# Performance work log

Hardware: AMD Instinct MI355X
Metric: run time of the kernel (lower is better)

The kernel has to match this reference:

```python
import jax, jax.numpy as jnp
import numpy as np

N, E, F_IN, F_E, H, HEADS, NG = 50000, 300000, 16, 8, 64, 4, 64
D_HEAD = H // HEADS
EPS = 1e-5


def setup_inputs() -> dict:
    key = jax.random.key(0)
    ks = jax.random.split(key, 12)
    def rn(k, shape, s=0.1):
        return jax.random.normal(k, shape, jnp.float32) * s
    return dict(
        x=jax.random.normal(ks[0], (N, F_IN), jnp.float32),
        edge_index=jax.random.randint(ks[1], (2, E), 0, N),
        edge_attr=jax.random.normal(ks[2], (E, F_E), jnp.float32),
        batch=jnp.sort(jax.random.randint(ks[3], (N,), 0, NG)),
        # edge_net: Linear(F_E, H*F_IN) -> ReLU -> Linear(H*F_IN, H*F_IN)
        en_w1=rn(ks[4], (F_E, H * F_IN)), en_b1=jnp.zeros((H * F_IN,), jnp.float32),
        en_w2=rn(ks[5], (H * F_IN, H * F_IN)), en_b2=jnp.zeros((H * F_IN,), jnp.float32),
        # NNConv root weight + bias
        root_w=rn(ks[6], (F_IN, H)), conv1_b=jnp.zeros((H,), jnp.float32),
        norm1_w=jnp.ones((H,), jnp.float32), norm1_b=jnp.zeros((H,), jnp.float32),
        # GATConv: lin weight, attention vectors, bias
        gat_w=rn(ks[7], (H, H)),
        att_src=rn(ks[8], (HEADS, D_HEAD)), att_dst=rn(ks[9], (HEADS, D_HEAD)),
        gat_b=jnp.zeros((H,), jnp.float32),
        norm2_w=jnp.ones((H,), jnp.float32), norm2_b=jnp.zeros((H,), jnp.float32),
        lin_w=rn(ks[10], (H, 1)), lin_b=jnp.zeros((1,), jnp.float32),
    )


def _graph_layernorm(x, w, b):
    # PyG LayerNorm(mode='graph') with batch=None: scalar mean/std over ALL elems
    mu = x.mean()
    sd = jnp.sqrt(((x - mu) ** 2).mean())
    return (x - mu) / (sd + EPS) * w + b


def reference(x, edge_index, edge_attr, batch, en_w1, en_b1, en_w2, en_b2,
              root_w, conv1_b, norm1_w, norm1_b, gat_w, att_src, att_dst,
              gat_b, norm2_w, norm2_b, lin_w, lin_b):
    src, dst = edge_index[0], edge_index[1]
    # --- NNConv: per-edge weight matrices from edge_net ---
    w_e = jax.nn.relu(edge_attr @ en_w1 + en_b1) @ en_w2 + en_b2
    w_e = w_e.reshape(E, F_IN, H)                      # [E, in, out]
    msg = jnp.einsum('ef,efh->eh', x[src], w_e)        # gather-matmul per edge
    agg = jax.ops.segment_sum(msg, dst, num_segments=N)
    deg = jax.ops.segment_sum(jnp.ones((E,), x.dtype), dst, num_segments=N)
    agg = agg / jnp.maximum(deg, 1.0)[:, None]         # aggr='mean'
    h = x @ root_w + agg + conv1_b
    h = jax.nn.relu(h)
    h = _graph_layernorm(h, norm1_w, norm1_b)
    # dropout: eval mode -> identity
    # --- GATConv (edge_attr=None at call site; add self-loops, softmax attn) ---
    loops = jnp.arange(N)
    s2 = jnp.concatenate([src, loops])
    d2 = jnp.concatenate([dst, loops])
    xh = (h @ gat_w).reshape(N, HEADS, D_HEAD)
    a_src = (xh * att_src).sum(-1)                     # [N, HEADS]
    a_dst = (xh * att_dst).sum(-1)
    alpha = jax.nn.leaky_relu(a_src[s2] + a_dst[d2], 0.2)  # [E+N, HEADS]
    amax = jax.ops.segment_max(alpha, d2, num_segments=N)
    alpha = jnp.exp(alpha - amax[d2])
    asum = jax.ops.segment_sum(alpha, d2, num_segments=N)
    alpha = alpha / (asum[d2] + 1e-16)
    out = jax.ops.segment_sum(alpha[:, :, None] * xh[s2], d2, num_segments=N)
    h2 = out.reshape(N, H) + gat_b                     # concat heads
    h2 = jax.nn.relu(h2)
    h2 = _graph_layernorm(h2, norm2_w, norm2_b)
    # --- global mean pool + linear head ---
    gs = jax.ops.segment_sum(h2, batch, num_segments=NG)
    cnt = jax.ops.segment_sum(jnp.ones((N,), h2.dtype), batch, num_segments=NG)
    pooled = gs / jnp.maximum(cnt, 1.0)[:, None]
    return pooled @ lin_w + lin_b                      # [NG, 1]
```

## Files before the change

### kernel.cpp

```cpp
#include <hip/hip_runtime.h>
#include <hip/hip_bf16.h>

#define N_NODES 50000
#define E_EDGES 300000
#define NGRAPH 64
#define NCHUNK 129
#define CSPLIT 65
#define NKG 1034
#define NEGRP 1172
#define LNEPS 1e-5f
#define NBLK_N 196
#define NBLK_P 12500
#define RPRE16 1.00048828125f

typedef _Float16 f16x8 __attribute__((ext_vector_type(8)));
typedef _Float16 f16x2 __attribute__((ext_vector_type(2)));
typedef float floatx16 __attribute__((ext_vector_type(16)));
typedef float f32x2 __attribute__((ext_vector_type(2)));
typedef unsigned int u32x4 __attribute__((ext_vector_type(4)));

__device__ __forceinline__ void async_load16(const void* g, void* l) {
  __builtin_amdgcn_global_load_lds(
      (__attribute__((address_space(1))) void*)g,
      (__attribute__((address_space(3))) void*)l, 16, 0, 0);
}

__global__ void k_prep(const float* __restrict__ w2, const float* __restrict__ b2,
                       _Float16* __restrict__ Tt3) {
  __shared__ float tile[32][65];
  int t = threadIdx.x;
  int kg0 = blockIdx.x * 2;
  int kf0 = kg0 * 16;
  int kfr = t >> 6;
  int n0 = t & 63;
#pragma unroll
  for (int it = 0; it < 8; ++it) {
    int kfl = it * 4 + kfr;
    int kf = kf0 + kfl;
    float v = 0.f;
    if (kf < 16384) v = w2[(size_t)kf * 64 + n0];
    else if (kf < 16400) v = b2[(size_t)(kf - 16384) * 64 + n0];
    tile[kfl][n0] = v;
  }
  __syncthreads();
  int kgl = t >> 7;
  int half = (t >> 6) & 1;
  int n = t & 63;
  f16x8 pack;
#pragma unroll
  for (int j = 0; j < 8; ++j) pack[j] = (_Float16)tile[kgl * 16 + half * 8 + j][n];
  *(f16x8*)(Tt3 + (size_t)(kg0 + kgl) * 1024 + half * 512 + n * 8) = pack;
}

__global__ void k_prepw(const float* __restrict__ w1, float* __restrict__ W1t) {
  int i = blockIdx.x * 256 + threadIdx.x;
  if (i < 8192) { int k = i >> 3, j = i & 7; W1t[i] = w1[j * 1024 + k]; }
}

__global__ void k_cnt(const int* __restrict__ ei, int* __restrict__ degI) {
  int e = blockIdx.x * 256 + threadIdx.x;
  if (e < E_EDGES) atomicAdd(&degI[ei[E_EDGES + e]], 1);
}

__global__ void k_scanA(const int* __restrict__ degI, int* __restrict__ bsum) {
  __shared__ int sm[256];
  int t = threadIdx.x;
  int i = blockIdx.x * 256 + t;
  sm[t] = (i < N_NODES) ? degI[i] : 0;
  __syncthreads();
  for (int off = 128; off > 0; off >>= 1) {
    if (t < off) sm[t] += sm[t + off];
    __syncthreads();
  }
  if (t == 0) bsum[blockIdx.x] = sm[0];
}

__global__ void k_scanB(const int* __restrict__ bsum, int* __restrict__ bpre) {
  __shared__ int s[256];
  int t = threadIdx.x;
  int v = (t < NBLK_N) ? bsum[t] : 0;
  s[t] = v;
  __syncthreads();
  for (int off = 1; off < 256; off <<= 1) {
    int add = (t >= off) ? s[t - off] : 0;
    __syncthreads();
    s[t] += add;
    __syncthreads();
  }
  if (t < NBLK_N) bpre[t] = s[t] - v;
}

__global__ void k_scanC(const int* __restrict__ degI, const int* __restrict__ bpre,
                        int* __restrict__ rowptr, int* __restrict__ cursor) {
  __shared__ int s[256];
  int t = threadIdx.x;
  int i = blockIdx.x * 256 + t;
  int d = (i < N_NODES) ? degI[i] : 0;
  s[t] = d;
  __syncthreads();
  for (int off = 1; off < 256; off <<= 1) {
    int add = (t >= off) ? s[t - off] : 0;
    __syncthreads();
    s[t] += add;
    __syncthreads();
  }
  int r = bpre[blockIdx.x] + s[t] - d;
  if (i < N_NODES) {
    rowptr[i] = r;
    cursor[i] = r;
    if (i == N_NODES - 1) rowptr[N_NODES] = r + d;
  }
}

__global__ void k_scatter(const int* __restrict__ ei, int* __restrict__ cursor,
                          int* __restrict__ colsrc) {
  int e = blockIdx.x * 256 + threadIdx.x;
  if (e < E_EDGES) {
    int s = ei[e], d = ei[E_EDGES + e];
    int pos = atomicAdd(&cursor[d], 1);
    colsrc[pos] = s;
  }
}

__global__ __launch_bounds__(256, 3)
void k_nnconv(const float* __restrict__ x, const int* __restrict__ ei,
              const float* __restrict__ ea, const float* __restrict__ W1t,
              const float* __restrict__ b1, const _Float16* __restrict__ Tt3,
              float* __restrict__ agg) {
  __shared__ __align__(16) _Float16 sB[2][8192];
  const int tid = threadIdx.x;
  const int wv = tid >> 6;
  const int lane = tid & 63;
  const int l31 = lane & 31;
  const int half = lane >> 5;
  const int grp = blockIdx.x >> 1;
  const int piece = blockIdx.x & 1;
  const int cstart = piece ? CSPLIT : 0;
  const int cend = piece ? NCHUNK : CSPLIT;

  int e = grp * 256 + tid;
  bool valid = e < E_EDGES;
  int srcv = valid ? ei[e] : 0;
  int dstv = valid ? ei[E_EDGES + e] : -1;

  f32x2 ea2[4];
  {
    const float4* p = (const float4*)(ea + (size_t)(valid ? e : 0) * 8);
    float4 a0 = p[0], a1 = p[1];
    ea2[0] = (f32x2){a0.x, a0.y};
    ea2[1] = (f32x2){a0.z, a0.w};
    ea2[2] = (f32x2){a1.x, a1.y};
    ea2[3] = (f32x2){a1.z, a1.w};
  }

  const int f0 = half * 8;
  unsigned xh16[2][4];
#pragma unroll
  for (int mt = 0; mt < 2; ++mt) {
    int s = __shfl(srcv, mt * 32 + l31);
    const float4* px = (const float4*)(x + (size_t)s * 16 + f0);
    float4 v0 = px[0], v1 = px[1];
    xh16[mt][0] = __builtin_bit_cast(unsigned, __builtin_amdgcn_cvt_pkrtz(v0.x * RPRE16, v0.y * RPRE16));
    xh16[mt][1] = __builtin_bit_cast(unsigned, __builtin_amdgcn_cvt_pkrtz(v0.z * RPRE16, v0.w * RPRE16));
    xh16[mt][2] = __builtin_bit_cast(unsigned, __builtin_amdgcn_cvt_pkrtz(v1.x * RPRE16, v1.y * RPRE16));
    xh16[mt][3] = __builtin_bit_cast(unsigned, __builtin_amdgcn_cvt_pkrtz(v1.z * RPRE16, v1.w * RPRE16));
  }

  int bpaddr[2];
#pragma unroll
  for (int mt = 0; mt < 2; ++mt) bpaddr[mt] = (mt * 32 + l31) * 4;

  const int loff = half * 512 + l31 * 8;

  auto stage = [&](int c, int nb) {
    const _Float16* src = Tt3 + ((size_t)c * 8 + 2 * wv) * 1024 + lane * 8;
    _Float16* dst = &sB[nb][2 * wv * 1024 + lane * 8];
    async_load16(src, dst);
    async_load16(src + 512, dst + 512);
    async_load16(src + 1024, dst + 1024);
    async_load16(src + 1536, dst + 1536);
  };

  unsigned prr[4];
  auto calcR = [&](int c, const float* w1p, const float* b1p) {
    if (c < 128) {
#pragma unroll
      for (int p = 0; p < 4; ++p) {
        float rv[2];
#pragma unroll
        for (int kk = 0; kk < 2; ++kk) {
          const f32x2* w = (const f32x2*)(w1p + (p * 2 + kk) * 8);
          f32x2 s01 = ea2[0] * w[0] + ea2[1] * w[1];
          f32x2 s23 = ea2[2] * w[2] + ea2[3] * w[3];
          f32x2 s = s01 + s23;
          rv[kk] = fmaxf(b1p[p * 2 + kk] + s[0] + s[1], 0.f) * RPRE16;
        }
        prr[p] = __builtin_bit_cast(unsigned, __builtin_amdgcn_cvt_pkrtz(rv[0], rv[1]));
      }
    } else {
      prr[0] = 0x00003C00u;
      prr[1] = prr[2] = prr[3] = 0u;
    }
  };

  unsigned ubuf[8];
  auto bcastR = [&]() {
#pragma unroll
    for (int p = 0; p < 4; ++p)
#pragma unroll
      for (int mt = 0; mt < 2; ++mt)
        ubuf[p * 2 + mt] = (unsigned)__builtin_amdgcn_ds_bpermute(bpaddr[mt], (int)prr[p]);
  };

  floatx16 acc[2][2];
#pragma unroll
  for (int mt = 0; mt < 2; ++mt)
#pragma unroll
    for (int nt = 0; nt < 2; ++nt)
#pragma unroll
      for (int r = 0; r < 16; ++r) acc[mt][nt][r] = 0.f;

  calcR(cstart, W1t + cstart * 64, b1 + cstart * 8);
  bcastR();
  stage(cstart, 0);
  __syncthreads();
  const float* w1p = W1t + (cstart + 1) * 64;
  const float* b1p = b1 + (cstart + 1) * 8;

  int c = cstart;
  int buf = 0;
  while (true) {
    unsigned rsp[16];
#pragma unroll
    for (int p = 0; p < 4; ++p)
#pragma unroll
      for (int mt = 0; mt < 2; ++mt) {
        unsigned u = ubuf[p * 2 + mt];
        rsp[(2 * p) * 2 + mt]     = __builtin_amdgcn_perm(u, 0u, 0x05040504u);
        rsp[(2 * p + 1) * 2 + mt] = __builtin_amdgcn_perm(u, 0u, 0x07060706u);
      }
    bool more = (c + 1 < cend);
    if (more) stage(c + 1, buf ^ 1);
    if (more) {
      calcR(c + 1, w1p, b1p);
      bcastR();
      w1p += 64; b1p += 8;
    }
    {
      f16x8 Bs0[2], Bs1[2];
      Bs0[0] = *(const f16x8*)&sB[buf][loff];
      Bs0[1] = *(const f16x8*)&sB[buf][loff + 256];
#pragma unroll
      for (int kg = 0; kg < 8; ++kg) {
        f16x8* cur = (kg & 1) ? Bs1 : Bs0;
        f16x8* nxt = (kg & 1) ? Bs0 : Bs1;
        if (kg < 7) {
          nxt[0] = *(const f16x8*)&sB[buf][(kg + 1) * 1024 + loff];
          nxt[1] = *(const f16x8*)&sB[buf][(kg + 1) * 1024 + loff + 256];
        }
#pragma unroll
        for (int mt = 0; mt < 2; ++mt) {
          f16x2 r2 = __builtin_bit_cast(f16x2, rsp[kg * 2 + mt]);
          u32x4 U;
#pragma unroll
          for (int j = 0; j < 4; ++j)
            U[j] = __builtin_bit_cast(unsigned,
                     __builtin_bit_cast(f16x2, xh16[mt][j]) * r2);
          f16x8 A = __builtin_bit_cast(f16x8, U);
#pragma unroll
          for (int nt = 0; nt < 2; ++nt)
            acc[mt][nt] = __builtin_amdgcn_mfma_f32_32x32x16_f16(A, cur[nt], acc[mt][nt], 0, 0, 0);
        }
      }
    }
    if (!more) break;
    __syncthreads();
    buf ^= 1;
    ++c;
  }

#pragma unroll
  for (int mt = 0; mt < 2; ++mt) {
#pragma unroll
    for (int reg = 0; reg < 16; ++reg) {
      int el = mt * 32 + (reg & 3) + 8 * (reg >> 2) + 4 * half;
      int dd = __shfl(dstv, el);
      if (dd >= 0) {
#pragma unroll
        for (int nt = 0; nt < 2; ++nt)
          atomicAdd(&agg[(size_t)dd * 64 + nt * 32 + l31], acc[mt][nt][reg]);
      }
    }
  }
}

__global__ void k_root(const float* __restrict__ x, const float* __restrict__ rootw,
                       const float* __restrict__ conv1b, const float* __restrict__ agg,
                       const int* __restrict__ degI, float* __restrict__ hpre,
                       float* __restrict__ rpart) {
  __shared__ float sW[1024];
  __shared__ float sx[64];
  __shared__ float red[8];
  int t = threadIdx.x;
  int blk = blockIdx.x;
#pragma unroll
  for (int i = 0; i < 4; ++i) sW[t + i * 256] = rootw[t + i * 256];
  if (t < 64) sx[t] = x[(size_t)blk * 64 + t];
  __syncthreads();
  int ln = t >> 6, h = t & 63;
  int n = blk * 4 + ln;
  float acc = conv1b[h];
#pragma unroll
  for (int f = 0; f < 16; ++f) acc += sx[ln * 16 + f] * sW[f * 64 + h];
  float dv = fmaxf((float)degI[n], 1.0f);
  float v = acc + agg[(size_t)n * 64 + h] / dv;
  v = fmaxf(v, 0.f);
  hpre[(size_t)n * 64 + h] = v;
  float s1 = v, s2 = v * v;
  for (int o = 32; o > 0; o >>= 1) { s1 += __shfl_down(s1, o); s2 += __shfl_down(s2, o); }
  if ((t & 63) == 0) { red[t >> 6] = s1; red[4 + (t >> 6)] = s2; }
  __syncthreads();
  if (t == 0) {
    rpart[blk * 2] = red[0] + red[1] + red[2] + red[3];
    rpart[blk * 2 + 1] = red[4] + red[5] + red[6] + red[7];
  }
}

__global__ void k_fold1(const float* __restrict__ rpart, const float* __restrict__ n1w,
                        const float* __restrict__ n1b, const float* __restrict__ gatw,
                        float* __restrict__ gw2, float* __restrict__ tb) {
  __shared__ float red[8];
  __shared__ float sMI[2];
  __shared__ float sS[64], sT[64];
  int t = threadIdx.x;
  int wv = t >> 6, lane = t & 63;
  float a = 0.f, b = 0.f;
  for (int i = t; i < NBLK_P; i += 256) { a += rpart[2 * i]; b += rpart[2 * i + 1]; }
  for (int o = 32; o > 0; o >>= 1) { a += __shfl_down(a, o); b += __shfl_down(b, o); }
  if (lane == 0) { red[wv] = a; red[4 + wv] = b; }
  __syncthreads();
  if (t == 0) {
    float A = red[0] + red[1] + red[2] + red[3];
    float B = red[4] + red[5] + red[6] + red[7];
    const float M = (float)N_NODES * 64.f;
    float mu = A / M;
    float var = fmaxf(B / M - mu * mu, 0.f);
    sMI[0] = mu;
    sMI[1] = 1.f / (sqrtf(var) + LNEPS);
  }
  __syncthreads();
  if (t < 64) {
    float mu = sMI[0], inv = sMI[1];
    sS[t] = inv * n1w[t];
    sT[t] = n1b[t] - mu * inv * n1w[t];
  }
  __syncthreads();
  if (t < 64) {
    float acc = 0.f;
    for (int i = 0; i < 64; ++i) {
      float g = gatw[i * 64 + t];
      gw2[i * 64 + t] = sS[i] * g;
      acc += sT[i] * g;
    }
    tb[t] = acc;
  }
}

__global__ void k_gatlin(const float* __restrict__ hpre, const float* __restrict__ gw2,
                         const float* __restrict__ tb, const float* __restrict__ attS,
                         const float* __restrict__ attD, float* __restrict__ xh,
                         float* __restrict__ asrc, float* __restrict__ adst) {
  __shared__ float sW[4096];
  __shared__ float sh[256];
  __shared__ float sxh[256];
  int t = threadIdx.x;
  int blk = blockIdx.x;
#pragma unroll
  for (int i = 0; i < 16; ++i) sW[t + i * 256] = gw2[t + i * 256];
  sh[t] = hpre[(size_t)blk * 256 + t];
  __syncthreads();
  int ln = t >> 6, h = t & 63;
  float acc = tb[h];
  for (int i = 0; i < 64; ++i) acc += sh[ln * 64 + i] * sW[i * 64 + h];
  xh[(size_t)blk * 256 + t] = acc;
  sxh[t] = acc;
  __syncthreads();
  if (t < 32) {
    int ln2 = t >> 3, rem = t & 7;
    int hd = rem & 3;
    const float* av = (rem >> 2) ? attD : attS;
    float a = 0.f;
#pragma unroll
    for (int d = 0; d < 16; ++d) a += sxh[ln2 * 64 + hd * 16 + d] * av[hd * 16 + d];
    int n = blk * 4 + ln2;
    if (rem >> 2) adst[n * 4 + hd] = a; else asrc[n * 4 + hd] = a;
  }
}

__global__ void k_gat(const int* __restrict__ rowptr, const int* __restrict__ colsrc,
                      const float* __restrict__ xh, const float* __restrict__ asrc,
                      const float* __restrict__ adst, const float* __restrict__ gatb,
                      float* __restrict__ act, float* __restrict__ gpart) {
  __shared__ float sP[4][256];
  __shared__ int sS[4][64];
  __shared__ float sRed[8];
  int t = threadIdx.x;
  int wv = t >> 6, lane = t & 63;
  int n = blockIdx.x * 4 + wv;
  int start = rowptr[n], end = rowptr[n + 1];
  int deg = end - start;
  int myhd = lane >> 4;
  float ad[4];
#pragma unroll
  for (int hd = 0; hd < 4; ++hd) ad[hd] = adst[n * 4 + hd];
  float m[4] = {-1e30f, -1e30f, -1e30f, -1e30f};
  float l[4] = {0.f, 0.f, 0.f, 0.f};
  float O = 0.f;
  int items = deg + 1;
  for (int t0 = 0; t0 < items; t0 += 64) {
    int cnt = min(64, items - t0);
    int idx = t0 + lane;
    bool has = lane < cnt;
    int s = n;
    if (has && idx < deg) s = colsrc[start + idx];
    float a[4];
#pragma unroll
    for (int hd = 0; hd < 4; ++hd) {
      float av = has ? (asrc[s * 4 + hd] + ad[hd]) : -1e30f;
      a[hd] = (av > 0.f) ? av : 0.2f * av;
    }
    float tm[4];
#pragma unroll
    for (int hd = 0; hd < 4; ++hd) tm[hd] = a[hd];
#pragma unroll
    for (int off = 32; off > 0; off >>= 1)
#pragma unroll
      for (int hd = 0; hd < 4; ++hd) tm[hd] = fmaxf(tm[hd], __shfl_xor(tm[hd], off));
    float p[4];
#pragma unroll
    for (int hd = 0; hd < 4; ++hd) {
      float mn = fmaxf(m[hd], tm[hd]);
      float sc = __expf(m[hd] - mn);
      l[hd] *= sc;
      if (hd == myhd) O *= sc;
      m[hd] = mn;
      p[hd] = has ? __expf(a[hd] - mn) : 0.f;
    }
    float ts[4];
#pragma unroll
    for (int hd = 0; hd < 4; ++hd) ts[hd] = p[hd];
#pragma unroll
    for (int off = 32; off > 0; off >>= 1)
#pragma unroll
      for (int hd = 0; hd < 4; ++hd) ts[hd] += __shfl_xor(ts[hd], off);
#pragma unroll
    for (int hd = 0; hd < 4; ++hd) l[hd] += ts[hd];
    sS[wv][lane] = s;
#pragma unroll
    for (int hd = 0; hd < 4; ++hd) sP[wv][lane * 4 + hd] = p[hd];
    for (int e2 = 0; e2 < cnt; ++e2) {
      int ss = sS[wv][e2];
      float pp = sP[wv][e2 * 4 + myhd];
      O = fmaf(pp, xh[(size_t)ss * 64 + lane], O);
    }
  }
  float lmy = (myhd & 2) ? ((myhd & 1) ? l[3] : l[2]) : ((myhd & 1) ? l[1] : l[0]);
  float outv = O / (lmy + 1e-16f);
  float v = fmaxf(outv + gatb[lane], 0.f);
  act[(size_t)n * 64 + lane] = v;
  float s1 = v, s2 = v * v;
#pragma unroll
  for (int off = 32; off > 0; off >>= 1) { s1 += __shfl_down(s1, off); s2 += __shfl_down(s2, off); }
  if (lane == 0) { sRed[wv] = s1; sRed[4 + wv] = s2; }
  __syncthreads();
  if (t == 0) {
    gpart[blockIdx.x * 2] = sRed[0] + sRed[1] + sRed[2] + sRed[3];
    gpart[blockIdx.x * 2 + 1] = sRed[4] + sRed[5] + sRed[6] + sRed[7];
  }
}

__global__ void k_fold2(const float* __restrict__ gpart, const float* __restrict__ n2w,
                        const float* __restrict__ n2b, const float* __restrict__ linw,
                        const float* __restrict__ linb, float* __restrict__ wl) {
  __shared__ float red[8];
  __shared__ float sMI[2];
  int t = threadIdx.x;
  int wv = t >> 6, lane = t & 63;
  float a = 0.f, b = 0.f;
  for (int i = t; i < NBLK_P; i += 256) { a += gpart[2 * i]; b += gpart[2 * i + 1]; }
  for (int o = 32; o > 0; o >>= 1) { a += __shfl_down(a, o); b += __shfl_down(b, o); }
  if (lane == 0) { red[wv] = a; red[4 + wv] = b; }
  __syncthreads();
  if (t == 0) {
    float A = red[0] + red[1] + red[2] + red[3];
    float B = red[4] + red[5] + red[6] + red[7];
    const float M = (float)N_NODES * 64.f;
    float mu = A / M;
    float var = fmaxf(B / M - mu * mu, 0.f);
    sMI[0] = mu;
    sMI[1] = 1.f / (sqrtf(var) + LNEPS);
  }
  __syncthreads();
  if (t < 64) {
    float mu = sMI[0], inv = sMI[1];
    float w = inv * n2w[t] * linw[t];
    float p = (n2b[t] - mu * inv * n2w[t]) * linw[t];
    wl[t] = w;
    for (int o = 32; o > 0; o >>= 1) p += __shfl_down(p, o);
    if (t == 0) wl[64] = p + linb[0];
  }
}

__global__ void k_out(const float* __restrict__ act, const float* __restrict__ wl,
                      const int* __restrict__ batch, float* __restrict__ out) {
  __shared__ float red[4];
  __shared__ float swl[64];
  int g = blockIdx.x;
  int t = threadIdx.x;
  int wv = t >> 6, lane = t & 63;
  if (t < 64) swl[t] = wl[t];
  __syncthreads();
  auto lbound = [&](int key) {
    int lo = 0, hi = N_NODES;
    while (lo < hi) { int mid = (lo + hi) >> 1; if (batch[mid] < key) lo = mid + 1; else hi = mid; }
    return lo;
  };
  int lo = lbound(g), hi = lbound(g + 1);
  int cntn = hi - lo;
  float s = 0.f;
  for (int idx = t; idx < cntn * 64; idx += 256) {
    int n = lo + (idx >> 6);
    int d = idx & 63;
    s += act[(size_t)n * 64 + d] * swl[d];
  }
  for (int o = 32; o > 0; o >>= 1) s += __shfl_down(s, o);
  if (lane == 0) red[wv] = s;
  __syncthreads();
  if (t == 0)
    out[g] = (red[0] + red[1] + red[2] + red[3]) / fmaxf((float)cntn, 1.f) + wl[64];
}

#define OFF_AGG     0UL
#define OFF_DEGI    12800000UL
#define ZBYTES      13000000UL
#define OFF_RPART   13000000UL
#define OFF_GPART   13100032UL
#define OFF_ROWPTR  13200064UL
#define OFF_CURSOR  13400128UL
#define OFF_BSUM    13600192UL
#define OFF_BPRE    13601024UL
#define OFF_COLSRC  13601856UL
#define OFF_TT      14801856UL
#define OFF_W1T     16923584UL
#define OFF_GW2     16956352UL
#define OFF_TB      16972736UL
#define OFF_WL      16972992UL
#define OFF_ASRC    16973312UL
#define OFF_ADST    17773312UL
#define OFF_HPRE    18573312UL
#define OFF_XH      31373312UL
#define OFF_ACT     44173312UL
#define WS_NEED     56973312UL

extern "C" void kernel_launch(void* const* d_in, const int* in_sizes, int n_in,
                              void* d_out, int out_size, void* d_ws, size_t ws_size,
                              hipStream_t stream) {
  const float* x = (const float*)d_in[0];
  const int* ei = (const int*)d_in[1];
  const float* ea = (const float*)d_in[2];
  const int* batch = (const int*)d_in[3];
  const float* w1 = (const float*)d_in[4];
  const float* b1 = (const float*)d_in[5];
  const float* w2 = (const float*)d_in[6];
  const float* b2 = (const float*)d_in[7];
  const float* rootw = (const float*)d_in[8];
  const float* conv1b = (const float*)d_in[9];
  const float* n1w = (const float*)d_in[10];
  const float* n1b = (const float*)d_in[11];
  const float* gatw = (const float*)d_in[12];
  const float* attS = (const float*)d_in[13];
  const float* attD = (const float*)d_in[14];
  const float* gatb = (const float*)d_in[15];
  const float* n2w = (const float*)d_in[16];
  const float* n2b = (const float*)d_in[17];
  const float* linw = (const float*)d_in[18];
  const float* linb = (const float*)d_in[19];

  if (ws_size < WS_NEED) return;
  char* ws = (char*)d_ws;
  float* agg    = (float*)(ws + OFF_AGG);
  int* degI     = (int*)(ws + OFF_DEGI);
  float* rpart  = (float*)(ws + OFF_RPART);
  float* gpart  = (float*)(ws + OFF_GPART);
  int* rowptr   = (int*)(ws + OFF_ROWPTR);
  int* cursor   = (int*)(ws + OFF_CURSOR);
  int* bsum     = (int*)(ws + OFF_BSUM);
  int* bpre     = (int*)(ws + OFF_BPRE);
  int* colsrc   = (int*)(ws + OFF_COLSRC);
  _Float16* Tt3 = (_Float16*)(ws + OFF_TT);
  float* W1t    = (float*)(ws + OFF_W1T);
  float* gw2    = (float*)(ws + OFF_GW2);
  float* tb     = (float*)(ws + OFF_TB);
  float* wl     = (float*)(ws + OFF_WL);
  float* asrc   = (float*)(ws + OFF_ASRC);
  float* adst   = (float*)(ws + OFF_ADST);
  float* hpre   = (float*)(ws + OFF_HPRE);
  float* xh     = (float*)(ws + OFF_XH);
  float* act    = (float*)(ws + OFF_ACT);

  hipMemsetAsync(ws, 0, ZBYTES, stream);

  k_prep<<<(NKG + 1) / 2, 256, 0, stream>>>(w2, b2, Tt3);
  k_prepw<<<32, 256, 0, stream>>>(w1, W1t);
  k_cnt<<<(E_EDGES + 255) / 256, 256, 0, stream>>>(ei, degI);
  k_scanA<<<NBLK_N, 256, 0, stream>>>(degI, bsum);
  k_scanB<<<1, 256, 0, stream>>>(bsum, bpre);
  k_scanC<<<NBLK_N, 256, 0, stream>>>(degI, bpre, rowptr, cursor);
  k_scatter<<<(E_EDGES + 255) / 256, 256, 0, stream>>>(ei, cursor, colsrc);
  k_nnconv<<<NEGRP * 2, 256, 0, stream>>>(x, ei, ea, W1t, b1, Tt3, agg);
  k_root<<<NBLK_P, 256, 0, stream>>>(x, rootw, conv1b, agg, degI, hpre, rpart);
  k_fold1<<<1, 256, 0, stream>>>(rpart, n1w, n1b, gatw, gw2, tb);
  k_gatlin<<<NBLK_P, 256, 0, stream>>>(hpre, gw2, tb, attS, attD, xh, asrc, adst);
  k_gat<<<NBLK_P, 256, 0, stream>>>(rowptr, colsrc, xh, asrc, adst, gatb, act, gpart);
  k_fold2<<<1, 256, 0, stream>>>(gpart, n2w, n2b, linw, linb, wl);
  k_out<<<NGRAPH, 256, 0, stream>>>(act, wl, batch, (float*)d_out);
}
```

Baseline: 914.3 us.

## Drop chunk split in NNConv, deepen B prefetch, fuse weight prep kernels

Result: slower. 935.3 us (+2.3%).

```diff
diff --git a/kernel.cpp b/kernel.cpp
--- a/kernel.cpp
+++ b/kernel.cpp
@@ -5,8 +5,7 @@
 #define E_EDGES 300000
 #define NGRAPH 64
 #define NCHUNK 129
-#define CSPLIT 65
-#define NKG 1034
+#define NKG 1032
 #define NEGRP 1172
 #define LNEPS 1e-5f
 #define NBLK_N 196
@@ -26,9 +25,17 @@
 }
 
 __global__ void k_prep(const float* __restrict__ w2, const float* __restrict__ b2,
-                       _Float16* __restrict__ Tt3) {
+                       const float* __restrict__ w1, _Float16* __restrict__ Tt3,
+                       float* __restrict__ W1t) {
+  int t = threadIdx.x;
+  if (blockIdx.x == NKG / 2) {
+    for (int i = t; i < 8192; i += 256) {
+      int k = i >> 3, j = i & 7;
+      W1t[i] = w1[j * 1024 + k];
+    }
+    return;
+  }
   __shared__ float tile[32][65];
-  int t = threadIdx.x;
   int kg0 = blockIdx.x * 2;
   int kf0 = kg0 * 16;
   int kfr = t >> 6;
@@ -50,11 +57,6 @@
 #pragma unroll
   for (int j = 0; j < 8; ++j) pack[j] = (_Float16)tile[kgl * 16 + half * 8 + j][n];
   *(f16x8*)(Tt3 + (size_t)(kg0 + kgl) * 1024 + half * 512 + n * 8) = pack;
-}
-
-__global__ void k_prepw(const float* __restrict__ w1, float* __restrict__ W1t) {
-  int i = blockIdx.x * 256 + threadIdx.x;
-  if (i < 8192) { int k = i >> 3, j = i & 7; W1t[i] = w1[j * 1024 + k]; }
 }
 
 __global__ void k_cnt(const int* __restrict__ ei, int* __restrict__ degI) {
@@ -133,12 +135,8 @@
   const int lane = tid & 63;
   const int l31 = lane & 31;
   const int half = lane >> 5;
-  const int grp = blockIdx.x >> 1;
-  const int piece = blockIdx.x & 1;
-  const int cstart = piece ? CSPLIT : 0;
-  const int cend = piece ? NCHUNK : CSPLIT;
-
-  int e = grp * 256 + tid;
+
+  int e = blockIdx.x * 256 + tid;
   bool valid = e < E_EDGES;
   int srcv = valid ? ei[e] : 0;
   int dstv = valid ? ei[E_EDGES + e] : -1;
@@ -220,16 +218,18 @@
 #pragma unroll
       for (int r = 0; r < 16; ++r) acc[mt][nt][r] = 0.f;
 
-  calcR(cstart, W1t + cstart * 64, b1 + cstart * 8);
+  calcR(0, W1t, b1);
   bcastR();
-  stage(cstart, 0);
-  __syncthreads();
-  const float* w1p = W1t + (cstart + 1) * 64;
-  const float* b1p = b1 + (cstart + 1) * 8;
-
-  int c = cstart;
+  stage(0, 0);
+  __syncthreads();
+  const float* w1p = W1t + 64;
+  const float* b1p = b1 + 8;
+
+  int c = 0;
   int buf = 0;
   while (true) {
+    bool more = (c + 1 < NCHUNK);
+    if (more) stage(c + 1, buf ^ 1);
     unsigned rsp[16];
 #pragma unroll
     for (int p = 0; p < 4; ++p)
@@ -239,24 +239,23 @@
         rsp[(2 * p) * 2 + mt]     = __builtin_amdgcn_perm(u, 0u, 0x05040504u);
         rsp[(2 * p + 1) * 2 + mt] = __builtin_amdgcn_perm(u, 0u, 0x07060706u);
       }
-    bool more = (c + 1 < cend);
-    if (more) stage(c + 1, buf ^ 1);
     if (more) {
       calcR(c + 1, w1p, b1p);
-      bcastR();
       w1p += 64; b1p += 8;
     }
     {
-      f16x8 Bs0[2], Bs1[2];
-      Bs0[0] = *(const f16x8*)&sB[buf][loff];
-      Bs0[1] = *(const f16x8*)&sB[buf][loff + 256];
+      f16x8 Bs[3][2];
+      Bs[0][0] = *(const f16x8*)&sB[buf][loff];
+      Bs[0][1] = *(const f16x8*)&sB[buf][loff + 256];
+      Bs[1][0] = *(const f16x8*)&sB[buf][1024 + loff];
+      Bs[1][1] = *(const f16x8*)&sB[buf][1024 + loff + 256];
 #pragma unroll
       for (int kg = 0; kg < 8; ++kg) {
-        f16x8* cur = (kg & 1) ? Bs1 : Bs0;
-        f16x8* nxt = (kg & 1) ? Bs0 : Bs1;
-        if (kg < 7) {
-          nxt[0] = *(const f16x8*)&sB[buf][(kg + 1) * 1024 + loff];
-          nxt[1] = *(const f16x8*)&sB[buf][(kg + 1) * 1024 + loff + 256];
+        int cs = kg % 3;
+        if (kg < 6) {
+          int ns = (kg + 2) % 3;
+          Bs[ns][0] = *(const f16x8*)&sB[buf][(kg + 2) * 1024 + loff];
+          Bs[ns][1] = *(const f16x8*)&sB[buf][(kg + 2) * 1024 + loff + 256];
         }
 #pragma unroll
         for (int mt = 0; mt < 2; ++mt) {
@@ -269,11 +268,12 @@
           f16x8 A = __builtin_bit_cast(f16x8, U);
 #pragma unroll
           for (int nt = 0; nt < 2; ++nt)
-            acc[mt][nt] = __builtin_amdgcn_mfma_f32_32x32x16_f16(A, cur[nt], acc[mt][nt], 0, 0, 0);
+            acc[mt][nt] = __builtin_amdgcn_mfma_f32_32x32x16_f16(A, Bs[cs][nt], acc[mt][nt], 0, 0, 0);
         }
       }
     }
     if (!more) break;
+    bcastR();
     __syncthreads();
     buf ^= 1;
     ++c;
@@ -551,16 +551,16 @@
 #define OFF_BPRE    13601024UL
 #define OFF_COLSRC  13601856UL
 #define OFF_TT      14801856UL
-#define OFF_W1T     16923584UL
-#define OFF_GW2     16956352UL
-#define OFF_TB      16972736UL
-#define OFF_WL      16972992UL
-#define OFF_ASRC    16973312UL
-#define OFF_ADST    17773312UL
-#define OFF_HPRE    18573312UL
-#define OFF_XH      31373312UL
-#define OFF_ACT     44173312UL
-#define WS_NEED     56973312UL
+#define OFF_W1T     16915392UL
+#define OFF_GW2     16948160UL
+#define OFF_TB      16964544UL
+#define OFF_WL      16964800UL
+#define OFF_ASRC    16965120UL
+#define OFF_ADST    17765120UL
+#define OFF_HPRE    18565120UL
+#define OFF_XH      31365120UL
+#define OFF_ACT     44165120UL
+#define WS_NEED     56965120UL
 
 extern "C" void kernel_launch(void* const* d_in, const int* in_sizes, int n_in,
                               void* d_out, int out_size, void* d_ws, size_t ws_size,
@@ -610,14 +610,13 @@
 
   hipMemsetAsync(ws, 0, ZBYTES, stream);
 
-  k_prep<<<(NKG + 1) / 2, 256, 0, stream>>>(w2, b2, Tt3);
-  k_prepw<<<32, 256, 0, stream>>>(w1, W1t);
+  k_prep<<<NKG / 2 + 1, 256, 0, stream>>>(w2, b2, w1, Tt3, W1t);
   k_cnt<<<(E_EDGES + 255) / 256, 256, 0, stream>>>(ei, degI);
   k_scanA<<<NBLK_N, 256, 0, stream>>>(degI, bsum);
   k_scanB<<<1, 256, 0, stream>>>(bsum, bpre);
   k_scanC<<<NBLK_N, 256, 0, stream>>>(degI, bpre, rowptr, cursor);
   k_scatter<<<(E_EDGES + 255) / 256, 256, 0, stream>>>(ei, cursor, colsrc);
-  k_nnconv<<<NEGRP * 2, 256, 0, stream>>>(x, ei, ea, W1t, b1, Tt3, agg);
+  k_nnconv<<<NEGRP, 256, 0, stream>>>(x, ei, ea, W1t, b1, Tt3, agg);
   k_root<<<NBLK_P, 256, 0, stream>>>(x, rootw, conv1b, agg, degI, hpre, rpart);
   k_fold1<<<1, 256, 0, stream>>>(rpart, n1w, n1b, gatw, gw2, tb);
   k_gatlin<<<NBLK_P, 256, 0, stream>>>(hpre, gw2, tb, attS, attD, xh, asrc, adst);
```
